# Optimization experiments

Hardware: AMD Instinct MI355X
Metric: run time of the kernel (lower is better)

## Reference

```python
import jax, jax.numpy as jnp
import numpy as np

LOG2 = np.float32(np.log(2.0))

def _jsd_pos(p):
    # get_positive_expectation, measure='JSD', average=False
    return LOG2 - jax.nn.softplus(-p)

def setup_inputs() -> dict:
    key = jax.random.key(0)
    k1, k2, k3, k4, k5, k6 = jax.random.split(key, 6)
    N, G, D = 65536, 512, 256
    batch_1 = jnp.sort(jax.random.randint(k1, (N,), 0, G))
    batch_2 = jnp.sort(jax.random.randint(k2, (N,), 0, G))
    z1 = jax.random.normal(k3, (N, D), dtype=jnp.float32)
    z2 = jax.random.normal(k4, (N, D), dtype=jnp.float32)
    g1 = jax.random.normal(k5, (G, D), dtype=jnp.float32)
    g2 = jax.random.normal(k6, (G, D), dtype=jnp.float32)
    return {"batch_1": batch_1, "batch_2": batch_2, "z1": z1, "z2": z2, "g1": g1, "g2": g2}

def reference(batch_1, batch_2, z1, z2, g1, g2):
    # pos_mask scatter-build -> dense one-hot [N, G]
    pos_mask_1 = jax.nn.one_hot(batch_1, g1.shape[0], dtype=z1.dtype)
    pos_mask_2 = jax.nn.one_hot(batch_2, g2.shape[0], dtype=z2.dtype)
    # masked node-graph similarity matrices [N, G]
    self_sim_1 = (z1 @ g1.T) * pos_mask_1
    self_sim_2 = (z2 @ g2.T) * pos_mask_2
    cross_sim_12 = (z1 @ g2.T) * pos_mask_1
    cross_sim_21 = (z2 @ g1.T) * pos_mask_2
    # sep=True branch: per-node row sums, L2 distance over nodes
    self_js_11 = _jsd_pos(self_sim_1).sum(1)
    cross_js_12 = _jsd_pos(cross_sim_12).sum(1)
    self_js_22 = _jsd_pos(self_sim_2).sum(1)
    cross_js_21 = _jsd_pos(cross_sim_21).sum(1)
    L_1 = jnp.sqrt(jnp.sum((self_js_11 - cross_js_12) ** 2))
    L_2 = jnp.sqrt(jnp.sum((self_js_22 - cross_js_21) ** 2))
    return L_1 + L_2
```

## Files before the change

### kernel.cpp

```cpp
#include <hip/hip_runtime.h>
#include <math.h>

__device__ __forceinline__ float spn(float p) {
    return fmaxf(-p, 0.0f) + __logf(1.0f + __expf(-fabsf(p)));
}

__device__ __forceinline__ float dot4(float4 a, float4 b) {
    return a.x * b.x + a.y * b.y + a.z * b.z + a.w * b.w;
}

__device__ __forceinline__ float wave64_reduce(float x) {
    int t;
    t = __builtin_amdgcn_update_dpp(0, __builtin_bit_cast(int, x), 0x111, 0xf, 0xf, true);
    x += __builtin_bit_cast(float, t);
    t = __builtin_amdgcn_update_dpp(0, __builtin_bit_cast(int, x), 0x112, 0xf, 0xf, true);
    x += __builtin_bit_cast(float, t);
    t = __builtin_amdgcn_update_dpp(0, __builtin_bit_cast(int, x), 0x114, 0xf, 0xf, true);
    x += __builtin_bit_cast(float, t);
    t = __builtin_amdgcn_update_dpp(0, __builtin_bit_cast(int, x), 0x118, 0xf, 0xf, true);
    x += __builtin_bit_cast(float, t);
    t = __builtin_amdgcn_update_dpp(0, __builtin_bit_cast(int, x), 0x142, 0xa, 0xf, true);
    x += __builtin_bit_cast(float, t);
    t = __builtin_amdgcn_update_dpp(0, __builtin_bit_cast(int, x), 0x143, 0xc, 0xf, true);
    x += __builtin_bit_cast(float, t);
    return x;
}

#define NBLOCKS 2048
#define NPW 8

__global__ __launch_bounds__(256) void jsd_dot_kernel(
    const int*   __restrict__ b1,
    const int*   __restrict__ b2,
    const float* __restrict__ z1,
    const float* __restrict__ z2,
    const float* __restrict__ g1,
    const float* __restrict__ g2,
    float*       __restrict__ partials)
{
    const int wave = threadIdx.x >> 6;
    const int lane = threadIdx.x & 63;
    const int w    = blockIdx.x * 4 + wave;

    const int sbase = __builtin_amdgcn_readfirstlane(w * NPW);

    int i1[NPW], i2[NPW];
    #pragma unroll
    for (int j = 0; j < NPW; ++j) {
        i1[j] = b1[sbase + j];
        i2[j] = b2[sbase + j];
    }

    const float4 w11c = ((const float4*)(g1 + (size_t)i1[0] * 256))[lane];
    const float4 w12c = ((const float4*)(g2 + (size_t)i1[0] * 256))[lane];
    const float4 w22c = ((const float4*)(g2 + (size_t)i2[0] * 256))[lane];
    const float4 w21c = ((const float4*)(g1 + (size_t)i2[0] * 256))[lane];

    float4 a1[NPW], a2[NPW];
    #pragma unroll
    for (int j = 0; j < NPW; ++j) {
        a1[j] = ((const float4*)(z1 + (size_t)(sbase + j) * 256))[lane];
        a2[j] = ((const float4*)(z2 + (size_t)(sbase + j) * 256))[lane];
    }

    float acc1 = 0.0f, acc2 = 0.0f;

    #pragma unroll
    for (int j = 0; j < NPW; ++j) {
        float4 v11 = w11c, v12 = w12c, v22 = w22c, v21 = w21c;
        if (i1[j] != i1[0]) {
            v11 = ((const float4*)(g1 + (size_t)i1[j] * 256))[lane];
            v12 = ((const float4*)(g2 + (size_t)i1[j] * 256))[lane];
        }
        if (i2[j] != i2[0]) {
            v22 = ((const float4*)(g2 + (size_t)i2[j] * 256))[lane];
            v21 = ((const float4*)(g1 + (size_t)i2[j] * 256))[lane];
        }

        float s11 = wave64_reduce(dot4(a1[j], v11));
        float c12 = wave64_reduce(dot4(a1[j], v12));
        float s22 = wave64_reduce(dot4(a2[j], v22));
        float c21 = wave64_reduce(dot4(a2[j], v21));

        if (lane == 63) {
            float d1 = spn(c12) - spn(s11);
            float d2 = spn(c21) - spn(s22);
            acc1 += d1 * d1;
            acc2 += d2 * d2;
        }
    }

    __shared__ float s1[4], s2[4];
    if (lane == 63) { s1[wave] = acc1; s2[wave] = acc2; }
    __syncthreads();

    if (threadIdx.x == 0) {
        partials[blockIdx.x * 2 + 0] = s1[0] + s1[1] + s1[2] + s1[3];
        partials[blockIdx.x * 2 + 1] = s2[0] + s2[1] + s2[2] + s2[3];
    }
}

__global__ __launch_bounds__(256) void jsd_reduce_kernel(
    const float* __restrict__ partials,
    float*       __restrict__ out)
{
    const int tid  = threadIdx.x;
    const int wave = tid >> 6;
    const int lane = tid & 63;

    float a = 0.0f, b = 0.0f;
    #pragma unroll
    for (int i = 0; i < NBLOCKS / 256; ++i) {
        a += partials[(i * 256 + tid) * 2 + 0];
        b += partials[(i * 256 + tid) * 2 + 1];
    }

    a = wave64_reduce(a);
    b = wave64_reduce(b);

    __shared__ float s1[4], s2[4];
    if (lane == 63) { s1[wave] = a; s2[wave] = b; }
    __syncthreads();

    if (tid == 0) {
        float t1 = s1[0] + s1[1] + s1[2] + s1[3];
        float t2 = s2[0] + s2[1] + s2[2] + s2[3];
        out[0] = sqrtf(t1) + sqrtf(t2);
    }
}

extern "C" void kernel_launch(void* const* d_in, const int* in_sizes, int n_in,
                              void* d_out, int out_size, void* d_ws, size_t ws_size,
                              hipStream_t stream) {
    const int*   b1 = (const int*)  d_in[0];
    const int*   b2 = (const int*)  d_in[1];
    const float* z1 = (const float*)d_in[2];
    const float* z2 = (const float*)d_in[3];
    const float* g1 = (const float*)d_in[4];
    const float* g2 = (const float*)d_in[5];
    float* out      = (float*)d_out;
    float* partials = (float*)d_ws;

    jsd_dot_kernel<<<NBLOCKS, 256, 0, stream>>>(b1, b2, z1, z2, g1, g2, partials);
    jsd_reduce_kernel<<<1, 256, 0, stream>>>(partials, out);
}
```

Before: 159.3 us.

## Stage z rows into LDS via global_load_lds and shrink per-wave work

The z1/z2 rows are now copied asynchronously into shared memory with global_load_lds rather than loaded into registers. Per-wave rows drop from 8 to 4 and the block count doubles to 4096. The g-row reuse shortcut is removed, so g rows are always loaded, relying on cache hits. The aim is to lower register pressure and raise occupancy and bytes in flight, at the cost of 32KB of LDS per block and a block barrier.

```diff
diff --git a/kernel.cpp b/kernel.cpp
--- a/kernel.cpp
+++ b/kernel.cpp
@@ -26,8 +26,17 @@
     return x;
 }
 
-#define NBLOCKS 2048
-#define NPW 8
+typedef const void __attribute__((address_space(1)))* gas_ptr;
+typedef void       __attribute__((address_space(3)))* las_ptr;
+
+__device__ __forceinline__ void stage_row(const float* grow, float* lrow, int lane) {
+    __builtin_amdgcn_global_load_lds((gas_ptr)(grow + lane * 4), (las_ptr)lrow,
+                                     16, 0, 0);
+}
+
+#define NBLOCKS 4096
+#define NPB 16
+#define NPW 4
 
 __global__ __launch_bounds__(256) void jsd_dot_kernel(
     const int*   __restrict__ b1,
@@ -38,11 +47,19 @@
     const float* __restrict__ g2,
     float*       __restrict__ partials)
 {
+    __shared__ float zs1[NPB * 256];
+    __shared__ float zs2[NPB * 256];
+
     const int wave = threadIdx.x >> 6;
     const int lane = threadIdx.x & 63;
-    const int w    = blockIdx.x * 4 + wave;
 
-    const int sbase = __builtin_amdgcn_readfirstlane(w * NPW);
+    const int sbase = __builtin_amdgcn_readfirstlane(blockIdx.x * NPB + wave * NPW);
+
+    #pragma unroll
+    for (int j = 0; j < NPW; ++j) {
+        stage_row(z1 + (size_t)(sbase + j) * 256, &zs1[(wave * NPW + j) * 256], lane);
+        stage_row(z2 + (size_t)(sbase + j) * 256, &zs2[(wave * NPW + j) * 256], lane);
+    }
 
     int i1[NPW], i2[NPW];
     #pragma unroll
@@ -51,36 +68,24 @@
         i2[j] = b2[sbase + j];
     }
 
-    const float4 w11c = ((const float4*)(g1 + (size_t)i1[0] * 256))[lane];
-    const float4 w12c = ((const float4*)(g2 + (size_t)i1[0] * 256))[lane];
-    const float4 w22c = ((const float4*)(g2 + (size_t)i2[0] * 256))[lane];
-    const float4 w21c = ((const float4*)(g1 + (size_t)i2[0] * 256))[lane];
-
-    float4 a1[NPW], a2[NPW];
-    #pragma unroll
-    for (int j = 0; j < NPW; ++j) {
-        a1[j] = ((const float4*)(z1 + (size_t)(sbase + j) * 256))[lane];
-        a2[j] = ((const float4*)(z2 + (size_t)(sbase + j) * 256))[lane];
-    }
+    __syncthreads();
 
     float acc1 = 0.0f, acc2 = 0.0f;
 
     #pragma unroll
     for (int j = 0; j < NPW; ++j) {
-        float4 v11 = w11c, v12 = w12c, v22 = w22c, v21 = w21c;
-        if (i1[j] != i1[0]) {
-            v11 = ((const float4*)(g1 + (size_t)i1[j] * 256))[lane];
-            v12 = ((const float4*)(g2 + (size_t)i1[j] * 256))[lane];
-        }
-        if (i2[j] != i2[0]) {
-            v22 = ((const float4*)(g2 + (size_t)i2[j] * 256))[lane];
-            v21 = ((const float4*)(g1 + (size_t)i2[j] * 256))[lane];
-        }
+        const float4 a1 = ((const float4*)&zs1[(wave * NPW + j) * 256])[lane];
+        const float4 a2 = ((const float4*)&zs2[(wave * NPW + j) * 256])[lane];
 
-        float s11 = wave64_reduce(dot4(a1[j], v11));
-        float c12 = wave64_reduce(dot4(a1[j], v12));
-        float s22 = wave64_reduce(dot4(a2[j], v22));
-        float c21 = wave64_reduce(dot4(a2[j], v21));
+        const float4 v11 = ((const float4*)(g1 + (size_t)i1[j] * 256))[lane];
+        const float4 v12 = ((const float4*)(g2 + (size_t)i1[j] * 256))[lane];
+        const float4 v22 = ((const float4*)(g2 + (size_t)i2[j] * 256))[lane];
+        const float4 v21 = ((const float4*)(g1 + (size_t)i2[j] * 256))[lane];
+
+        float s11 = wave64_reduce(dot4(a1, v11));
+        float c12 = wave64_reduce(dot4(a1, v12));
+        float s22 = wave64_reduce(dot4(a2, v22));
+        float c21 = wave64_reduce(dot4(a2, v21));
 
         if (lane == 63) {
             float d1 = spn(c12) - spn(s11);
```

Measured after the change: 157.4 us. No clear change (-1.2%).
